# Performance work log

Measured on AMD Instinct MI355X. Metric: run time of the kernel, lower is better.

Reference implementation:

```python
import jax, jax.numpy as jnp
import numpy as np

N = 250_000          # total event nodes across the batch
E = 1_000_000        # directed edges (radius-graph style, avg degree 4)
B = 25               # graphs in the batch
BS = N // B          # nodes per graph (contiguous blocks)
NX, NY = 8, 9        # ceil(120/16), ceil(100/12) voxel cells for MaxPooling
NC = NX * NY         # 72 voxel cells per graph
M = B * NC           # pooled node slots (empty cells kept but masked)
GRIDS = 16           # MaxPoolingX: 4x4 cells of size (30,25) over 120x100
NOUT = 2
EPS = 1e-5


def spline_basis(p):
    # SplineConv basis: kernel_size=2 per dim, degree=1 open B-spline, dim=3.
    # basis_s(p) = prod_d (p_d if bit_d(s) else 1 - p_d), s = b0 + 2*b1 + 4*b2
    p = jnp.clip(p, 0.0, 1.0)
    cols = []
    for s in range(8):
        w = jnp.ones(p.shape[0], p.dtype)
        for d in range(3):
            w = w * (p[:, d] if (s >> d) & 1 else 1.0 - p[:, d])
        cols.append(w)
    return jnp.stack(cols, axis=1)  # [E, 8]


def spline_conv(x, src, dst, basis, W, emask, num_nodes):
    # SplineConv with aggr='mean', bias=False, root_weight=False
    xj = x[src]                                   # [E, Cin] gather
    msg = jnp.zeros((xj.shape[0], W.shape[2]), x.dtype)
    for s in range(W.shape[0]):                   # 8 kernel weight matrices
        msg = msg + basis[:, s:s + 1] * (xj @ W[s])
    msg = msg * emask[:, None]
    out = jax.ops.segment_sum(msg, dst, num_segments=num_nodes)
    deg = jax.ops.segment_sum(emask, dst, num_segments=num_nodes)
    return out / jnp.maximum(deg, 1.0)[:, None]


def batch_norm(x, gamma, beta, mask=None):
    # BatchNorm1d over nodes (training-mode batch statistics, biased var)
    if mask is None:
        mean = x.mean(axis=0)
        var = jnp.mean((x - mean) ** 2, axis=0)
        return (x - mean) * jax.lax.rsqrt(var + EPS) * gamma + beta
    m = mask.astype(x.dtype)[:, None]
    cnt = jnp.maximum(m.sum(), 1.0)
    mean = (x * m).sum(axis=0) / cnt
    var = (((x - mean) ** 2) * m).sum(axis=0) / cnt
    return ((x - mean) * jax.lax.rsqrt(var + EPS) * gamma + beta) * m


def _forward(x, pos, edge_attr, ws, gs, bs, fc_w, edge_index, batch):
    src, dst = edge_index[0], edge_index[1]
    basis = spline_basis(edge_attr)
    em = jnp.ones((src.shape[0],), x.dtype)
    for i in range(5):  # conv1..conv5 + norm + relu on the full event graph
        x = spline_conv(x, src, dst, basis, ws[i], em, N)
        x = jax.nn.relu(batch_norm(x, gs[i], bs[i]))
    # ---- MaxPooling: voxel grid (16,12) over pos[:, :2], coarsen graph ----
    cx = jnp.clip(jnp.floor(pos[:, 0] / 16.0).astype(jnp.int32), 0, NX - 1)
    cy = jnp.clip(jnp.floor(pos[:, 1] / 12.0).astype(jnp.int32), 0, NY - 1)
    cluster = batch * NC + cy * NX + cx           # [N] -> [0, M)
    cnt = jax.ops.segment_sum(jnp.ones((N,), x.dtype), cluster, num_segments=M)
    nmask = cnt > 0                               # non-empty voxel cells
    xp = jax.ops.segment_max(x, cluster, num_segments=M)
    xp = jnp.where(nmask[:, None], xp, 0.0)       # [M, 32]
    pp = jax.ops.segment_sum(pos, cluster, num_segments=M) / jnp.maximum(cnt, 1.0)[:, None]
    # coarsen edges: remap via cluster, drop self loops, coalesce duplicates
    key = cluster[src] * M + cluster[dst]
    key = jnp.where(cluster[src] == cluster[dst], M * M, key)
    ks = jnp.sort(key)
    dup = jnp.concatenate([jnp.zeros((1,), bool), ks[1:] == ks[:-1]])
    evalid = (ks < M * M) & (~dup)
    rs = jnp.where(evalid, ks // M, 0)
    cs = jnp.where(evalid, ks % M, 0)
    emf = evalid.astype(x.dtype)
    # Cartesian(norm=True, cat=False) on pooled positions
    d = (pp[cs] - pp[rs]) * emf[:, None]
    maxv = jnp.maximum(jnp.max(jnp.abs(d)), 1e-9)
    ea2 = d / (2.0 * maxv) + 0.5
    basis2 = spline_basis(ea2)
    for i in range(5, 7):  # conv6, conv7 on pooled graph
        xp = spline_conv(xp, rs, cs, basis2, ws[i], emf, M)
        xp = jax.nn.relu(batch_norm(xp, gs[i], bs[i], nmask))
    # ---- MaxPoolingX: (30,25) voxel grid -> 4x4 = 16 cells per graph ----
    bcl = jnp.arange(M, dtype=jnp.int32) // NC    # batch id of each cluster
    gx = jnp.clip(jnp.floor(pp[:, 0] / 30.0).astype(jnp.int32), 0, 3)
    gy = jnp.clip(jnp.floor(pp[:, 1] / 25.0).astype(jnp.int32), 0, 3)
    seg = jnp.where(nmask, bcl * GRIDS + gy * 4 + gx, B * GRIDS)
    xg = jax.ops.segment_max(xp, seg, num_segments=B * GRIDS + 1)[:B * GRIDS]
    xg = jnp.where(jnp.isfinite(xg), xg, 0.0)     # empty cells -> 0
    feat = xg.reshape(B, GRIDS * 32)              # [B, 512]
    return feat @ fc_w.T                          # [B, NOUT]


def setup_inputs() -> dict:
    key = jax.random.key(0)
    k = jax.random.split(key, 16)
    x = jax.random.uniform(k[0], (N, 1), dtype=jnp.float32)
    pos = jax.random.uniform(k[1], (N, 3), dtype=jnp.float32) * jnp.array([120.0, 100.0, 1.0], jnp.float32)
    batch = (jnp.arange(N) // BS).astype(jnp.int32)
    src = jax.random.randint(k[2], (E,), 0, N, dtype=jnp.int32)
    dst = (src // BS) * BS + jax.random.randint(k[3], (E,), 0, BS, dtype=jnp.int32)
    edge_index = jnp.stack([src, dst])
    edge_attr = jax.random.uniform(k[4], (E, 3), dtype=jnp.float32)
    chans = [1, 8, 16, 16, 16, 32, 32, 32]
    inp = {"x": x, "pos": pos, "edge_attr": edge_attr}
    for i in range(7):
        cin, cout = chans[i], chans[i + 1]
        inp[f"w{i+1}"] = jax.random.normal(k[5 + i], (8, cin, cout), jnp.float32) / np.sqrt(8.0 * cin)
    for i in range(7):
        inp[f"g{i+1}"] = jnp.ones((chans[i + 1],), jnp.float32)
    for i in range(7):
        inp[f"b{i+1}"] = jnp.zeros((chans[i + 1],), jnp.float32)
    inp["fc_w"] = jax.random.normal(k[12], (NOUT, GRIDS * 32), jnp.float32) * 0.05
    inp["edge_index"] = edge_index
    inp["batch"] = batch
    return inp


def reference(x, pos, edge_attr, w1, w2, w3, w4, w5, w6, w7,
              g1, g2, g3, g4, g5, g6, g7,
              b1, b2, b3, b4, b5, b6, b7, fc_w, edge_index, batch):
    ws = (w1, w2, w3, w4, w5, w6, w7)
    gs = (g1, g2, g3, g4, g5, g6, g7)
    bs = (b1, b2, b3, b4, b5, b6, b7)
    return _forward(x, pos, edge_attr, ws, gs, bs, fc_w, edge_index, batch)
```

## Files before the change

### kernel.cpp

```cpp
#include <hip/hip_runtime.h>

constexpr int NN   = 250000;
constexpr int NE   = 1000000;
constexpr int NBm  = 25;
constexpr int BSg  = NN / NBm;
constexpr int NCc  = 72;
constexpr int MM   = NBm * NCc;
constexpr int PRES = NBm * NCc * NCc;
constexpr int NBK  = NBm * 16;
constexpr float EPSbn = 1e-5f;


__global__ __launch_bounds__(256) void k_deg(const int* __restrict__ dst, int* __restrict__ deg, int n) {
    int e = blockIdx.x * 256 + threadIdx.x;
    if (e < n) atomicAdd(&deg[dst[e]], 1);
}

__global__ __launch_bounds__(256) void k_dhist(const int* __restrict__ deg, const int* __restrict__ batch,
                                               int* __restrict__ dhist, int n) {
    __shared__ int h[NBK];
    int tid = threadIdx.x;
    for (int i = tid; i < NBK; i += 256) h[i] = 0;
    __syncthreads();
    int i = blockIdx.x * 256 + tid;
    if (i < n) atomicAdd(&h[batch[i] * 16 + (15 - min(deg[i], 15))], 1);
    __syncthreads();
    for (int b = tid; b < NBK; b += 256) if (h[b]) atomicAdd(&dhist[b], h[b]);
}

__global__ __launch_bounds__(256) void k_dscan(const int* __restrict__ dhist, int* __restrict__ dcur) {
    __shared__ int tmp[NBK];
    int t = threadIdx.x;
    for (int i = t; i < NBK; i += 256) tmp[i] = dhist[i];
    __syncthreads();
    if (t == 0) { int run = 0; for (int i = 0; i < NBK; i++) { int v = tmp[i]; tmp[i] = run; run += v; } }
    __syncthreads();
    for (int i = t; i < NBK; i += 256) dcur[i] = tmp[i];
}

__global__ __launch_bounds__(256) void k_dscat(const int* __restrict__ deg, const int* __restrict__ batch,
                                               const float* __restrict__ x_in,
                                               int* __restrict__ dcur, int* __restrict__ pinv,
                                               int* __restrict__ deg_p, float* __restrict__ xin_p, int n) {
    __shared__ int lcnt[NBK];
    __shared__ int gbase[NBK];
    int tid = threadIdx.x;
    for (int i = tid; i < NBK; i += 256) lcnt[i] = 0;
    __syncthreads();
    int i = blockIdx.x * 256 + tid;
    int b = 0, rank = 0;
    if (i < n) {
        b = batch[i] * 16 + (15 - min(deg[i], 15));
        rank = atomicAdd(&lcnt[b], 1);
    }
    __syncthreads();
    for (int k = tid; k < NBK; k += 256)
        if (lcnt[k]) gbase[k] = atomicAdd(&dcur[k], lcnt[k]);
    __syncthreads();
    if (i < n) {
        int slot = gbase[b] + rank;
        pinv[i] = slot;
        deg_p[slot] = deg[i];
        xin_p[slot] = x_in[i];
    }
}

__global__ __launch_bounds__(256) void k_scan1(const int* __restrict__ in, int n,
                                               int* __restrict__ outEx, int* __restrict__ bsum) {
    __shared__ int lds[256];
    int t = threadIdx.x;
    int base = blockIdx.x * 2048;
    int v[8]; int s = 0;
#pragma unroll
    for (int i = 0; i < 8; i++) { int idx = base + t * 8 + i; v[i] = (idx < n) ? in[idx] : 0; s += v[i]; }
    lds[t] = s; __syncthreads();
    for (int o = 1; o < 256; o <<= 1) {
        int x = (t >= o) ? lds[t - o] : 0; __syncthreads();
        lds[t] += x; __syncthreads();
    }
    if (t == 255) bsum[blockIdx.x] = lds[255];
    int run = lds[t] - s;
#pragma unroll
    for (int i = 0; i < 8; i++) { int idx = base + t * 8 + i; if (idx < n) outEx[idx] = run; run += v[i]; }
}

__global__ __launch_bounds__(256) void k_scan2(int* bsum, int nb) {
    __shared__ int l[256];
    int t = threadIdx.x;
    int v = (t < nb) ? bsum[t] : 0;
    l[t] = v; __syncthreads();
    for (int o = 1; o < 256; o <<= 1) {
        int x = (t >= o) ? l[t - o] : 0; __syncthreads();
        l[t] += x; __syncthreads();
    }
    if (t < nb) bsum[t] = l[t] - v;
}

__global__ __launch_bounds__(256) void k_scan3(int* __restrict__ outEx, int n, const int* __restrict__ bsum) {
    int i = blockIdx.x * 256 + threadIdx.x;
    if (i < n) outEx[i] += bsum[i >> 11];
}

__global__ __launch_bounds__(256) void k_scatter(const int* __restrict__ src, const int* __restrict__ dst,
                                                 const float* __restrict__ ea, const int* __restrict__ offx,
                                                 const int* __restrict__ pinv,
                                                 int* __restrict__ cursor, float4* __restrict__ erec, int n) {
    int e = blockIdx.x * 256 + threadIdx.x;
    if (e >= n) return;
    int d = pinv[dst[e]];
    int j = offx[d] + atomicAdd(&cursor[d], 1);
    float p0 = fminf(fmaxf(ea[e * 3 + 0], 0.f), 1.f);
    float p1 = fminf(fmaxf(ea[e * 3 + 1], 0.f), 1.f);
    float p2 = fminf(fmaxf(ea[e * 3 + 2], 0.f), 1.f);
    erec[j] = make_float4(__int_as_float(pinv[src[e]]), p0, p1, p2);
}

__global__ __launch_bounds__(256) void k_cluster(const float* __restrict__ pos, const int* __restrict__ pinv,
                                                 int* __restrict__ cluster, int* __restrict__ cluster_p,
                                                 int* __restrict__ cnt, float* __restrict__ ppsum) {
    __shared__ int lcnt[NCc];
    __shared__ float lpp[NCc * 3];
    int tid = threadIdx.x;
    int g = blockIdx.x >> 3, part = blockIdx.x & 7;
    for (int i = tid; i < NCc; i += 256) lcnt[i] = 0;
    for (int i = tid; i < NCc * 3; i += 256) lpp[i] = 0.f;
    __syncthreads();
    int base = g * BSg + part * (BSg / 8);
    int lim = BSg / 8;
    for (int k = tid; k < lim; k += 256) {
        int i = base + k;
        float px = pos[i * 3], py = pos[i * 3 + 1], pz = pos[i * 3 + 2];
        int cx = min(max((int)floorf(px / 16.f), 0), 7);
        int cy = min(max((int)floorf(py / 12.f), 0), 8);
        int lc = cy * 8 + cx;
        cluster[i] = g * NCc + lc;
        cluster_p[pinv[i]] = g * NCc + lc;
        atomicAdd(&lcnt[lc], 1);
        atomicAdd(&lpp[lc * 3 + 0], px);
        atomicAdd(&lpp[lc * 3 + 1], py);
        atomicAdd(&lpp[lc * 3 + 2], pz);
    }
    __syncthreads();
    for (int c = tid; c < NCc; c += 256) {
        if (lcnt[c]) {
            atomicAdd(&cnt[g * NCc + c], lcnt[c]);
            atomicAdd(&ppsum[(g * NCc + c) * 3 + 0], lpp[c * 3 + 0]);
            atomicAdd(&ppsum[(g * NCc + c) * 3 + 1], lpp[c * 3 + 1]);
            atomicAdd(&ppsum[(g * NCc + c) * 3 + 2], lpp[c * 3 + 2]);
        }
    }
}

__global__ __launch_bounds__(256) void k_coarse(const int* __restrict__ src, const int* __restrict__ dst,
                                                const int* __restrict__ cluster, unsigned char* __restrict__ presence,
                                                int n) {
    int e = blockIdx.x * 256 + threadIdx.x;
    if (e >= n) return;
    int r = cluster[src[e]], c = cluster[dst[e]];
    if (r == c) return;
    int g = r / NCc;
    presence[g * (NCc * NCc) + (r % NCc) * NCc + (c % NCc)] = 1;
}

__global__ __launch_bounds__(256) void k_fpp(const int* __restrict__ cnt, const float* __restrict__ ppsum,
                                             float* __restrict__ pp, int* __restrict__ nmask, int* __restrict__ nmc) {
    int m = blockIdx.x * 256 + threadIdx.x;
    if (m >= MM) return;
    int c = cnt[m];
    float inv = 1.f / (float)max(c, 1);
    pp[m * 3 + 0] = ppsum[m * 3 + 0] * inv;
    pp[m * 3 + 1] = ppsum[m * 3 + 1] * inv;
    pp[m * 3 + 2] = ppsum[m * 3 + 2] * inv;
    nmask[m] = (c > 0);
    if (c > 0) atomicAdd(nmc, 1);
}

__global__ __launch_bounds__(256) void k_maxv(const unsigned char* __restrict__ presence, const float* __restrict__ pp,
                                              float* __restrict__ maxv) {
    int i = blockIdx.x * 256 + threadIdx.x;
    float m = 0.f;
    if (i < PRES && presence[i]) {
        int g = i / (NCc * NCc), rem = i % (NCc * NCc);
        int r = g * NCc + rem / NCc, c = g * NCc + rem % NCc;
        float d0 = fabsf(pp[c * 3 + 0] - pp[r * 3 + 0]);
        float d1 = fabsf(pp[c * 3 + 1] - pp[r * 3 + 1]);
        float d2 = fabsf(pp[c * 3 + 2] - pp[r * 3 + 2]);
        m = fmaxf(fmaxf(d0, d1), d2);
    }
    for (int o = 32; o; o >>= 1) m = fmaxf(m, __shfl_xor(m, o));
    if ((threadIdx.x & 63) == 0) atomicMax((int*)maxv, __float_as_int(m));
}


template <int CIN, int COUT, int TPN, bool BN>
__global__ __launch_bounds__(256) void k_conv(
    const float* __restrict__ x, const float4* __restrict__ erec,
    const int* __restrict__ off, const int* __restrict__ deg,
    const float* __restrict__ W, const float* __restrict__ st,
    const float* __restrict__ gam, const float* __restrict__ bet, float invcnt,
    float* __restrict__ out, float* __restrict__ stG, int nwaves) {
    constexpr int CPT = CIN / TPN;
    constexpr int SLICE = COUT + 4;
    constexpr int NPW = 128 / TPN;
    constexpr int CPG = (BSg + NPW - 1) / NPW;
    constexpr int WPG = (CPG + 1) / 2;
    constexpr int NH = (COUT > 16) ? 2 : 1;
    constexpr int OH = COUT / NH;
    constexpr int CWH = OH / TPN;
    __shared__ float Ws[8 * CIN * SLICE];
    __shared__ float ssum[COUT], ssq[COUT];
    int tid = threadIdx.x;
    for (int idx = tid; idx < 8 * CIN * COUT; idx += 256) {
        int s = idx / (CIN * COUT), r = idx % (CIN * COUT);
        int ci = r / COUT, co = r % COUT;
        int t_ = ci / CPT, i_ = ci % CPT;
        Ws[((s * CPT + i_) * TPN + t_) * SLICE + co] = W[idx];
    }
    if (tid < COUT) { ssum[tid] = 0.f; ssq[tid] = 0.f; }
    __syncthreads();

    int w = blockIdx.x * 4 + (tid >> 6);
    int lane = tid & 63;
    int t = lane & (TPN - 1);
    int qi = lane / TPN;
    bool wact = (w < nwaves);
    int g = wact ? (w / WPG) : 0;
    int p = wact ? (w % WPG) : 0;

    float sc[CPT], sh[CPT];
    if constexpr (BN) {
#pragma unroll
        for (int i = 0; i < CPT; i++) {
            int c = t * CPT + i;
            float mean = st[c] * invcnt;
            float var = st[CIN + c] * invcnt - mean * mean;
            float s = rsqrtf(var + EPSbn) * gam[c];
            sc[i] = s; sh[i] = bet[c] - mean * s;
        }
    }

    for (int rep = 0; rep < 2; rep++) {
        if (!wact) break;
        int c = rep ? (CPG - 1 - p) : p;
        if (rep && c == p) break;
        int base = g * BSg + c * NPW;
        int lim = min(NPW, BSg - c * NPW);
        int no = 2 * qi;
        bool act = no < lim;
        int n0 = base + no;

        float agg[2][8 * CPT];
#pragma unroll
        for (int r = 0; r < 2; r++)
#pragma unroll
            for (int i = 0; i < 8 * CPT; i++) agg[r][i] = 0.f;

        int dg0 = 0, dg1 = 0, jb0 = 0, jb1 = 0;
        if (act) {
            jb0 = off[n0];     dg0 = deg[n0];
            jb1 = off[n0 + 1]; dg1 = deg[n0 + 1];
        }
        int mx = max(dg0, dg1);
        int cl0 = max(dg0 - 1, 0), cl1 = max(dg1 - 1, 0);
        float4 rec0 = erec[min(jb0, NE - 1)];
        float4 rec1 = erec[min(jb1, NE - 1)];
        float4 nrec0 = erec[jb0 + min(1, cl0)];
        float4 nrec1 = erec[jb1 + min(1, cl1)];
        float xc0[CPT], xc1[CPT];
        {
            const float* xs0 = &x[(size_t)__float_as_int(rec0.x) * CIN + t * CPT];
            const float* xs1 = &x[(size_t)__float_as_int(rec1.x) * CIN + t * CPT];
            if constexpr (CPT == 4) {
                float4 v0 = *(const float4*)xs0; float4 v1 = *(const float4*)xs1;
                xc0[0] = v0.x; xc0[1] = v0.y; xc0[2] = v0.z; xc0[3] = v0.w;
                xc1[0] = v1.x; xc1[1] = v1.y; xc1[2] = v1.z; xc1[3] = v1.w;
            } else if constexpr (CPT == 8) {
#pragma unroll
                for (int i = 0; i < 8; i += 4) {
                    float4 v0 = *(const float4*)&xs0[i]; float4 v1 = *(const float4*)&xs1[i];
                    xc0[i] = v0.x; xc0[i + 1] = v0.y; xc0[i + 2] = v0.z; xc0[i + 3] = v0.w;
                    xc1[i] = v1.x; xc1[i + 1] = v1.y; xc1[i + 2] = v1.z; xc1[i + 3] = v1.w;
                }
            } else {
#pragma unroll
                for (int i = 0; i < CPT; i++) { xc0[i] = xs0[i]; xc1[i] = xs1[i]; }
            }
        }
        for (int m = 0; m < mx; m++) {
            float xn0[CPT], xn1[CPT];
            {
                const float* xs0 = &x[(size_t)__float_as_int(nrec0.x) * CIN + t * CPT];
                const float* xs1 = &x[(size_t)__float_as_int(nrec1.x) * CIN + t * CPT];
                if constexpr (CPT == 4) {
                    float4 v0 = *(const float4*)xs0; float4 v1 = *(const float4*)xs1;
                    xn0[0] = v0.x; xn0[1] = v0.y; xn0[2] = v0.z; xn0[3] = v0.w;
                    xn1[0] = v1.x; xn1[1] = v1.y; xn1[2] = v1.z; xn1[3] = v1.w;
                } else if constexpr (CPT == 8) {
#pragma unroll
                    for (int i = 0; i < 8; i += 4) {
                        float4 v0 = *(const float4*)&xs0[i]; float4 v1 = *(const float4*)&xs1[i];
                        xn0[i] = v0.x; xn0[i + 1] = v0.y; xn0[i + 2] = v0.z; xn0[i + 3] = v0.w;
                        xn1[i] = v1.x; xn1[i + 1] = v1.y; xn1[i + 2] = v1.z; xn1[i + 3] = v1.w;
                    }
                } else {
#pragma unroll
                    for (int i = 0; i < CPT; i++) { xn0[i] = xs0[i]; xn1[i] = xs1[i]; }
                }
            }
            float4 nn0 = erec[jb0 + min(m + 2, cl0)];
            float4 nn1 = erec[jb1 + min(m + 2, cl1)];
            float f0 = (m < dg0) ? 1.f : 0.f;
            float f1 = (m < dg1) ? 1.f : 0.f;
            float xv0[CPT], xv1[CPT];
#pragma unroll
            for (int i = 0; i < CPT; i++) { xv0[i] = xc0[i]; xv1[i] = xc1[i]; }
            if constexpr (BN) {
#pragma unroll
                for (int i = 0; i < CPT; i++) {
                    float a = xv0[i] * sc[i] + sh[i]; xv0[i] = a > 0.f ? a : 0.f;
                    float b = xv1[i] * sc[i] + sh[i]; xv1[i] = b > 0.f ? b : 0.f;
                }
            }
            {
                float p0 = rec0.y, p1 = rec0.z;
                float p2 = rec0.w * f0, q2 = (1.f - rec0.w) * f0;
                float q0 = 1.f - p0, q1 = 1.f - p1;
                float a00 = q0 * q1, a10 = p0 * q1, a01 = q0 * p1, a11 = p0 * p1;
                float bbv[8] = {a00 * q2, a10 * q2, a01 * q2, a11 * q2,
                                a00 * p2, a10 * p2, a01 * p2, a11 * p2};
#pragma unroll
                for (int k = 0; k < 8; k++)
#pragma unroll
                    for (int i = 0; i < CPT; i++) agg[0][k * CPT + i] += bbv[k] * xv0[i];
            }
            {
                float p0 = rec1.y, p1 = rec1.z;
                float p2 = rec1.w * f1, q2 = (1.f - rec1.w) * f1;
                float q0 = 1.f - p0, q1 = 1.f - p1;
                float a00 = q0 * q1, a10 = p0 * q1, a01 = q0 * p1, a11 = p0 * p1;
                float bbv[8] = {a00 * q2, a10 * q2, a01 * q2, a11 * q2,
                                a00 * p2, a10 * p2, a01 * p2, a11 * p2};
#pragma unroll
                for (int k = 0; k < 8; k++)
#pragma unroll
                    for (int i = 0; i < CPT; i++) agg[1][k * CPT + i] += bbv[k] * xv1[i];
            }
            rec0 = nrec0; rec1 = nrec1;
            nrec0 = nn0; nrec1 = nn1;
#pragma unroll
            for (int i = 0; i < CPT; i++) { xc0[i] = xn0[i]; xc1[i] = xn1[i]; }
        }

        float inv0 = 1.f / (float)max(dg0, 1);
        float inv1 = 1.f / (float)max(dg1, 1);

#pragma unroll
        for (int h = 0; h < NH; h++) {
            float o0[OH], o1[OH];
#pragma unroll
            for (int c2 = 0; c2 < OH; c2++) { o0[c2] = 0.f; o1[c2] = 0.f; }
#pragma unroll
            for (int k = 0; k < 8; k++)
#pragma unroll
                for (int i = 0; i < CPT; i++) {
                    float a0 = agg[0][k * CPT + i];
                    float a1 = agg[1][k * CPT + i];
                    const float4* wr = (const float4*)&Ws[((k * CPT + i) * TPN + t) * SLICE + h * OH];
#pragma unroll
                    for (int c2 = 0; c2 < OH / 4; c2++) {
                        float4 wv = wr[c2];
                        o0[4 * c2 + 0] += a0 * wv.x; o0[4 * c2 + 1] += a0 * wv.y;
                        o0[4 * c2 + 2] += a0 * wv.z; o0[4 * c2 + 3] += a0 * wv.w;
                        o1[4 * c2 + 0] += a1 * wv.x; o1[4 * c2 + 1] += a1 * wv.y;
                        o1[4 * c2 + 2] += a1 * wv.z; o1[4 * c2 + 3] += a1 * wv.w;
                    }
                }
#pragma unroll
            for (int m = 1; m < TPN; m <<= 1)
#pragma unroll
                for (int c2 = 0; c2 < OH; c2++) { o0[c2] += __shfl_xor(o0[c2], m); o1[c2] += __shfl_xor(o1[c2], m); }

            float v0[CWH], v1[CWH], sv[CWH], qv[CWH];
#pragma unroll
            for (int c2 = 0; c2 < CWH; c2++) {
                v0[c2] = act ? o0[t * CWH + c2] * inv0 : 0.f;
                v1[c2] = act ? o1[t * CWH + c2] * inv1 : 0.f;
                sv[c2] = v0[c2] + v1[c2];
                qv[c2] = v0[c2] * v0[c2] + v1[c2] * v1[c2];
            }
            if (act) {
                float* op0 = &out[(size_t)n0 * COUT + h * OH + t * CWH];
                float* op1 = op0 + COUT;
#pragma unroll
                for (int c2 = 0; c2 < CWH; c2++) { op0[c2] = v0[c2]; op1[c2] = v1[c2]; }
            }
#pragma unroll
            for (int m = TPN; m < 64; m <<= 1)
#pragma unroll
                for (int c2 = 0; c2 < CWH; c2++) { sv[c2] += __shfl_xor(sv[c2], m); qv[c2] += __shfl_xor(qv[c2], m); }
            if (lane < TPN) {
#pragma unroll
                for (int c2 = 0; c2 < CWH; c2++) {
                    atomicAdd(&ssum[h * OH + t * CWH + c2], sv[c2]);
                    atomicAdd(&ssq[h * OH + t * CWH + c2], qv[c2]);
                }
            }
        }
    }
    __syncthreads();
    if (tid < COUT) atomicAdd(&stG[tid], ssum[tid]);
    else if (tid < 2 * COUT) atomicAdd(&stG[tid], ssq[tid - COUT]);
}

__global__ __launch_bounds__(256) void k_pool(const float* __restrict__ x, const int* __restrict__ cluster_p,
                                              const float* __restrict__ st, const float* __restrict__ gam,
                                              const float* __restrict__ bet, float invcnt,
                                              float* __restrict__ xp) {
    __shared__ float cellv[NCc * 32];
    __shared__ float scs[32], shs[32];
    int tid = threadIdx.x;
    int g = blockIdx.x >> 3, part = blockIdx.x & 7;
    for (int i = tid; i < NCc * 32; i += 256) cellv[i] = 0.f;
    if (tid < 32) {
        float mean = st[tid] * invcnt;
        float var = st[32 + tid] * invcnt - mean * mean;
        float s = rsqrtf(var + EPSbn) * gam[tid];
        scs[tid] = s; shs[tid] = bet[tid] - mean * s;
    }
    __syncthreads();
    int base = g * BSg + part * (BSg / 8);
    const int nelem = (BSg / 8) * 32;
    for (int ii = tid; ii < nelem; ii += 256) {
        int nd = base + (ii >> 5), ch = ii & 31;
        float v = x[(size_t)nd * 32 + ch] * scs[ch] + shs[ch];
        v = v > 0.f ? v : 0.f;
        int lc = cluster_p[nd] - g * NCc;
        atomicMax((int*)&cellv[lc * 32 + ch], __float_as_int(v));
    }
    __syncthreads();
    for (int ii = tid; ii < NCc * 32; ii += 256)
        atomicMax((int*)&xp[g * NCc * 32 + ii], __float_as_int(cellv[ii]));
}

__global__ __launch_bounds__(256) void k_y(const float* __restrict__ xp, const float* __restrict__ W,
                                           float* __restrict__ y) {
    int i = blockIdx.x * 256 + threadIdx.x;
    if (i >= MM * 256) return;
    int r = i >> 8, rem = i & 255, s = rem >> 5, co = rem & 31;
    const float* xr = &xp[r * 32];
    const float* w = &W[s * 1024 + co];
    float a = 0.f;
#pragma unroll
    for (int ci = 0; ci < 32; ci++) a += xr[ci] * w[ci * 32];
    y[i] = a;
}

__global__ __launch_bounds__(256) void k_y2(const float* __restrict__ pt, const float* __restrict__ W,
                                            const float* __restrict__ st, const float* __restrict__ gam,
                                            const float* __restrict__ bet, const int* __restrict__ nmask,
                                            const int* __restrict__ nmc, float* __restrict__ y) {
    __shared__ float scs[32], shs[32];
    int tid = threadIdx.x;
    if (tid < 32) {
        float cntf = (float)max(nmc[0], 1);
        float mean = st[tid] / cntf;
        float var = st[32 + tid] / cntf - mean * mean;
        float s = rsqrtf(var + EPSbn) * gam[tid];
        scs[tid] = s; shs[tid] = bet[tid] - mean * s;
    }
    __syncthreads();
    int i = blockIdx.x * 256 + tid;
    if (i >= MM * 256) return;
    int r = i >> 8, rem = i & 255, s = rem >> 5, co = rem & 31;
    float a = 0.f;
    if (nmask[r]) {
        const float* xr = &pt[r * 32];
        const float* w = &W[s * 1024 + co];
#pragma unroll
        for (int ci = 0; ci < 32; ci++) {
            float v = xr[ci] * scs[ci] + shs[ci];
            v = v > 0.f ? v : 0.f;
            a += v * w[ci * 32];
        }
    }
    y[i] = a;
}

__global__ __launch_bounds__(256) void k_convp(const float* __restrict__ y, const float* __restrict__ pp,
                                               const unsigned char* __restrict__ presence,
                                               const float* __restrict__ maxv, float* __restrict__ out,
                                               float* __restrict__ stG) {
    __shared__ float ssum[32], ssq[32];
    int tid = threadIdx.x;
    if (tid < 32) { ssum[tid] = 0.f; ssq[tid] = 0.f; }
    __syncthreads();
    int i = blockIdx.x * 256 + tid;
    int c = i >> 5, co = i & 31;
    int g = c / NCc, lc = c % NCc;
    float mv = fmaxf(maxv[0], 1e-9f);
    float inv2 = 0.5f / mv;
    float pcx = pp[c * 3], pcy = pp[c * 3 + 1], pcz = pp[c * 3 + 2];
    const unsigned char* pr = &presence[g * (NCc * NCc) + lc];
    float acc = 0.f; int dg = 0;
    for (int lr = 0; lr < NCc; lr++) {
        if (pr[lr * NCc]) {
            dg++;
            int r = g * NCc + lr;
            float p0 = fminf(fmaxf((pcx - pp[r * 3]) * inv2 + 0.5f, 0.f), 1.f);
            float p1 = fminf(fmaxf((pcy - pp[r * 3 + 1]) * inv2 + 0.5f, 0.f), 1.f);
            float p2 = fminf(fmaxf((pcz - pp[r * 3 + 2]) * inv2 + 0.5f, 0.f), 1.f);
            float q0 = 1.f - p0, q1 = 1.f - p1, q2 = 1.f - p2;
            const float* yr = &y[r * 256 + co];
            acc += (q0 * q1 * q2) * yr[0]   + (p0 * q1 * q2) * yr[32]
                 + (q0 * p1 * q2) * yr[64]  + (p0 * p1 * q2) * yr[96]
                 + (q0 * q1 * p2) * yr[128] + (p0 * q1 * p2) * yr[160]
                 + (q0 * p1 * p2) * yr[192] + (p0 * p1 * p2) * yr[224];
        }
    }
    float val = acc / (float)max(dg, 1);
    out[i] = val;
    float sv = val, qv = val * val;
    sv += __shfl_xor(sv, 32); qv += __shfl_xor(qv, 32);
    int lane = tid & 63;
    if (lane < 32) { atomicAdd(&ssum[lane], sv); atomicAdd(&ssq[lane], qv); }
    __syncthreads();
    if (tid < 32) atomicAdd(&stG[tid], ssum[tid]);
    else if (tid < 64) atomicAdd(&stG[32 + tid - 32], ssq[tid - 32]);
}

__global__ __launch_bounds__(256) void k_poolX(const float* __restrict__ pt, const float* __restrict__ pp,
                                               const float* __restrict__ st, const float* __restrict__ gam,
                                               const float* __restrict__ bet, const int* __restrict__ nmask,
                                               const int* __restrict__ nmc, float* __restrict__ xg) {
    int i = blockIdx.x * 256 + threadIdx.x;
    if (i >= MM * 32) return;
    int m = i >> 5, ch = i & 31;
    if (!nmask[m]) return;
    float cntf = (float)max(nmc[0], 1);
    float mean = st[ch] / cntf;
    float var = st[32 + ch] / cntf - mean * mean;
    float s = rsqrtf(var + EPSbn) * gam[ch];
    float v = pt[i] * s + (bet[ch] - mean * s);
    v = v > 0.f ? v : 0.f;
    int g = m / NCc;
    int gx = min(max((int)floorf(pp[m * 3] / 30.f), 0), 3);
    int gy = min(max((int)floorf(pp[m * 3 + 1] / 25.f), 0), 3);
    int seg = g * 16 + gy * 4 + gx;
    atomicMax((int*)&xg[seg * 32 + ch], __float_as_int(v));
}

__global__ __launch_bounds__(64) void k_fc(const float* __restrict__ xg, const float* __restrict__ fcw,
                                           float* __restrict__ out) {
    int q = blockIdx.x;
    int b = q >> 1, o = q & 1;
    int l = threadIdx.x;
    float a = 0.f;
    for (int k = l; k < 512; k += 64) a += xg[b * 512 + k] * fcw[o * 512 + k];
    for (int s = 32; s; s >>= 1) a += __shfl_xor(a, s);
    if (l == 0) out[b * 2 + o] = a;
}


extern "C" void kernel_launch(void* const* d_in, const int* in_sizes, int n_in,
                              void* d_out, int out_size, void* d_ws, size_t ws_size,
                              hipStream_t stream) {
    const float* x_in  = (const float*)d_in[0];
    const float* pos   = (const float*)d_in[1];
    const float* eattr = (const float*)d_in[2];
    const float* w[7];  for (int i = 0; i < 7; i++) w[i]  = (const float*)d_in[3 + i];
    const float* gm[7]; for (int i = 0; i < 7; i++) gm[i] = (const float*)d_in[10 + i];
    const float* bt[7]; for (int i = 0; i < 7; i++) bt[i] = (const float*)d_in[17 + i];
    const float* fcw   = (const float*)d_in[24];
    const int* ei      = (const int*)d_in[25];
    const int* batch   = (const int*)d_in[26];
    const int* esrc = ei;
    const int* edst = ei + NE;
    float* outp = (float*)d_out;

    char* base = (char*)d_ws;
    size_t cur = 0;
    auto alloc = [&](size_t elems) -> void* {
        void* p = base + cur;
        cur += (((elems * 4) + 255) & ~(size_t)255);
        return p;
    };
    int*   deg_i     = (int*)alloc(NN);
    int*   cursor    = (int*)alloc(NN);
    int*   cnt_i     = (int*)alloc(MM);
    float* ppsum     = (float*)alloc(MM * 3);
    unsigned char* presence = (unsigned char*)alloc(PRES / 4);
    float* maxv      = (float*)alloc(64);
    int*   nmc       = (int*)alloc(64);
    int*   dhist     = (int*)alloc(NBK);
    float* st        = (float*)alloc(7 * 64);
    float* xp_pool   = (float*)alloc(MM * 32);
    float* xg        = (float*)alloc(NBm * 16 * 32);
    size_t zero_bytes = cur;
    int*   off_ex    = (int*)alloc(NN);
    int*   bsum      = (int*)alloc(256);
    int*   cluster   = (int*)alloc(NN);
    int*   cluster_p = (int*)alloc(NN);
    int*   dcur      = (int*)alloc(NBK);
    int*   pinv      = (int*)alloc(NN);
    int*   deg_p     = (int*)alloc(NN);
    float* xin_p     = (float*)alloc(NN);
    float4* erec     = (float4*)alloc((size_t)NE * 4);
    float* x_a       = (float*)alloc((size_t)NN * 32);
    float* x_b       = (float*)alloc((size_t)NN * 16);
    float* pp        = (float*)alloc(MM * 3);
    int*   nmask     = (int*)alloc(MM);
    float* ybuf      = (float*)alloc(MM * 256);
    float* pt0       = (float*)alloc(MM * 32);
    float* pt1       = (float*)alloc(MM * 32);
    (void)ws_size; (void)in_sizes; (void)n_in; (void)out_size;

    (void)hipMemsetAsync(d_ws, 0, zero_bytes, stream);

    int gE = (NE + 255) / 256;
    int gN = (NN + 255) / 256;
    int nbS = (NN + 2047) / 2048;

    k_deg<<<gE, 256, 0, stream>>>(edst, deg_i, NE);
    k_dhist<<<gN, 256, 0, stream>>>(deg_i, batch, dhist, NN);
    k_dscan<<<1, 256, 0, stream>>>(dhist, dcur);
    k_dscat<<<gN, 256, 0, stream>>>(deg_i, batch, x_in, dcur, pinv, deg_p, xin_p, NN);
    k_scan1<<<nbS, 256, 0, stream>>>(deg_p, NN, off_ex, bsum);
    k_scan2<<<1, 256, 0, stream>>>(bsum, nbS);
    k_scan3<<<gN, 256, 0, stream>>>(off_ex, NN, bsum);
    k_scatter<<<gE, 256, 0, stream>>>(esrc, edst, eattr, off_ex, pinv, cursor, erec, NE);
    k_cluster<<<NBm * 8, 256, 0, stream>>>(pos, pinv, cluster, cluster_p, cnt_i, ppsum);
    k_coarse<<<gE, 256, 0, stream>>>(esrc, edst, cluster, presence, NE);
    k_fpp<<<(MM + 255) / 256, 256, 0, stream>>>(cnt_i, ppsum, pp, nmask, nmc);
    k_maxv<<<(PRES + 255) / 256, 256, 0, stream>>>(presence, pp, maxv);

    const float invN = 1.f / (float)NN;
    constexpr int W1 = NBm * ((((BSg + 127) / 128) + 1) / 2);
    constexpr int W2 = NBm * ((((BSg + 63) / 64) + 1) / 2);
    constexpr int W4 = NBm * ((((BSg + 31) / 32) + 1) / 2);
    k_conv<1, 8, 1, false><<<(W1 + 3) / 4, 256, 0, stream>>>(xin_p, erec, off_ex, deg_p,
                                                             w[0], nullptr, nullptr, nullptr, 0.f, x_a, st + 0, W1);
    k_conv<8, 16, 2, true><<<(W2 + 3) / 4, 256, 0, stream>>>(x_a, erec, off_ex, deg_p,
                                                             w[1], st + 0, gm[0], bt[0], invN, x_b, st + 64, W2);
    k_conv<16, 16, 4, true><<<(W4 + 3) / 4, 256, 0, stream>>>(x_b, erec, off_ex, deg_p,
                                                              w[2], st + 64, gm[1], bt[1], invN, x_a, st + 128, W4);
    k_conv<16, 16, 4, true><<<(W4 + 3) / 4, 256, 0, stream>>>(x_a, erec, off_ex, deg_p,
                                                              w[3], st + 128, gm[2], bt[2], invN, x_b, st + 192, W4);
    k_conv<16, 32, 4, true><<<(W4 + 3) / 4, 256, 0, stream>>>(x_b, erec, off_ex, deg_p,
                                                              w[4], st + 192, gm[3], bt[3], invN, x_a, st + 256, W4);
    k_pool<<<NBm * 8, 256, 0, stream>>>(x_a, cluster_p, st + 256, gm[4], bt[4], invN, xp_pool);
    k_y<<<(MM * 256 + 255) / 256, 256, 0, stream>>>(xp_pool, w[5], ybuf);
    k_convp<<<(MM * 32) / 256, 256, 0, stream>>>(ybuf, pp, presence, maxv, pt0, st + 320);
    k_y2<<<(MM * 256 + 255) / 256, 256, 0, stream>>>(pt0, w[6], st + 320, gm[5], bt[5], nmask, nmc, ybuf);
    k_convp<<<(MM * 32) / 256, 256, 0, stream>>>(ybuf, pp, presence, maxv, pt1, st + 384);
    k_poolX<<<(MM * 32 + 255) / 256, 256, 0, stream>>>(pt1, pp, st + 384, gm[6], bt[6], nmask, nmc, xg);
    k_fc<<<50, 64, 0, stream>>>(xg, fcw, outp);
}
```

Before: 630.0 us.

## Fuse edge scatter with coarse presence, shrink conv blocks, drop x prefetch

Merges the edge scatter and coarse-graph presence kernels into one pass over the edges, so src/dst are read once and one launch is removed. Halves the conv blocks to 128 threads (two waves each), which gives more blocks and spreads the shared weight staging, but each block now loads the weight tile for fewer waves. Removes the software pipelining of neighbor feature gathers in the conv loop. This lowers register pressure but exposes gather latency on every edge iteration.

```diff
diff --git a/kernel.cpp b/kernel.cpp
--- a/kernel.cpp
+++ b/kernel.cpp
@@ -99,20 +99,6 @@
 __global__ __launch_bounds__(256) void k_scan3(int* __restrict__ outEx, int n, const int* __restrict__ bsum) {
     int i = blockIdx.x * 256 + threadIdx.x;
     if (i < n) outEx[i] += bsum[i >> 11];
-}
-
-__global__ __launch_bounds__(256) void k_scatter(const int* __restrict__ src, const int* __restrict__ dst,
-                                                 const float* __restrict__ ea, const int* __restrict__ offx,
-                                                 const int* __restrict__ pinv,
-                                                 int* __restrict__ cursor, float4* __restrict__ erec, int n) {
-    int e = blockIdx.x * 256 + threadIdx.x;
-    if (e >= n) return;
-    int d = pinv[dst[e]];
-    int j = offx[d] + atomicAdd(&cursor[d], 1);
-    float p0 = fminf(fmaxf(ea[e * 3 + 0], 0.f), 1.f);
-    float p1 = fminf(fmaxf(ea[e * 3 + 1], 0.f), 1.f);
-    float p2 = fminf(fmaxf(ea[e * 3 + 2], 0.f), 1.f);
-    erec[j] = make_float4(__int_as_float(pinv[src[e]]), p0, p1, p2);
 }
 
 __global__ __launch_bounds__(256) void k_cluster(const float* __restrict__ pos, const int* __restrict__ pinv,
@@ -151,15 +137,25 @@
     }
 }
 
-__global__ __launch_bounds__(256) void k_coarse(const int* __restrict__ src, const int* __restrict__ dst,
-                                                const int* __restrict__ cluster, unsigned char* __restrict__ presence,
-                                                int n) {
+__global__ __launch_bounds__(256) void k_scatter(const int* __restrict__ src, const int* __restrict__ dst,
+                                                 const float* __restrict__ ea, const int* __restrict__ offx,
+                                                 const int* __restrict__ pinv, const int* __restrict__ cluster,
+                                                 int* __restrict__ cursor, float4* __restrict__ erec,
+                                                 unsigned char* __restrict__ presence, int n) {
     int e = blockIdx.x * 256 + threadIdx.x;
     if (e >= n) return;
-    int r = cluster[src[e]], c = cluster[dst[e]];
-    if (r == c) return;
-    int g = r / NCc;
-    presence[g * (NCc * NCc) + (r % NCc) * NCc + (c % NCc)] = 1;
+    int s = src[e], d = dst[e];
+    int pd = pinv[d];
+    int j = offx[pd] + atomicAdd(&cursor[pd], 1);
+    float p0 = fminf(fmaxf(ea[e * 3 + 0], 0.f), 1.f);
+    float p1 = fminf(fmaxf(ea[e * 3 + 1], 0.f), 1.f);
+    float p2 = fminf(fmaxf(ea[e * 3 + 2], 0.f), 1.f);
+    erec[j] = make_float4(__int_as_float(pinv[s]), p0, p1, p2);
+    int r = cluster[s], c = cluster[d];
+    if (r != c) {
+        int g = r / NCc;
+        presence[g * (NCc * NCc) + (r % NCc) * NCc + (c % NCc)] = 1;
+    }
 }
 
 __global__ __launch_bounds__(256) void k_fpp(const int* __restrict__ cnt, const float* __restrict__ ppsum,
@@ -193,7 +189,7 @@
 
 
 template <int CIN, int COUT, int TPN, bool BN>
-__global__ __launch_bounds__(256) void k_conv(
+__global__ __launch_bounds__(128) void k_conv(
     const float* __restrict__ x, const float4* __restrict__ erec,
     const int* __restrict__ off, const int* __restrict__ deg,
     const float* __restrict__ W, const float* __restrict__ st,
@@ -210,7 +206,7 @@
     __shared__ float Ws[8 * CIN * SLICE];
     __shared__ float ssum[COUT], ssq[COUT];
     int tid = threadIdx.x;
-    for (int idx = tid; idx < 8 * CIN * COUT; idx += 256) {
+    for (int idx = tid; idx < 8 * CIN * COUT; idx += 128) {
         int s = idx / (CIN * COUT), r = idx % (CIN * COUT);
         int ci = r / COUT, co = r % COUT;
         int t_ = ci / CPT, i_ = ci % CPT;
@@ -219,7 +215,7 @@
     if (tid < COUT) { ssum[tid] = 0.f; ssq[tid] = 0.f; }
     __syncthreads();
 
-    int w = blockIdx.x * 4 + (tid >> 6);
+    int w = blockIdx.x * 2 + (tid >> 6);
     int lane = tid & 63;
     int t = lane & (TPN - 1);
     int qi = lane / TPN;
@@ -264,56 +260,33 @@
         int cl0 = max(dg0 - 1, 0), cl1 = max(dg1 - 1, 0);
         float4 rec0 = erec[min(jb0, NE - 1)];
         float4 rec1 = erec[min(jb1, NE - 1)];
-        float4 nrec0 = erec[jb0 + min(1, cl0)];
-        float4 nrec1 = erec[jb1 + min(1, cl1)];
-        float xc0[CPT], xc1[CPT];
-        {
-            const float* xs0 = &x[(size_t)__float_as_int(rec0.x) * CIN + t * CPT];
-            const float* xs1 = &x[(size_t)__float_as_int(rec1.x) * CIN + t * CPT];
+        for (int m = 0; m < mx; m++) {
+            int s0 = __float_as_int(rec0.x);
+            int s1 = __float_as_int(rec1.x);
+            const float* xs0 = &x[(size_t)s0 * CIN + t * CPT];
+            const float* xs1 = &x[(size_t)s1 * CIN + t * CPT];
+            float xv0[CPT], xv1[CPT];
             if constexpr (CPT == 4) {
-                float4 v0 = *(const float4*)xs0; float4 v1 = *(const float4*)xs1;
-                xc0[0] = v0.x; xc0[1] = v0.y; xc0[2] = v0.z; xc0[3] = v0.w;
-                xc1[0] = v1.x; xc1[1] = v1.y; xc1[2] = v1.z; xc1[3] = v1.w;
+                float4 v0 = *(const float4*)xs0;
+                float4 v1 = *(const float4*)xs1;
+                xv0[0] = v0.x; xv0[1] = v0.y; xv0[2] = v0.z; xv0[3] = v0.w;
+                xv1[0] = v1.x; xv1[1] = v1.y; xv1[2] = v1.z; xv1[3] = v1.w;
             } else if constexpr (CPT == 8) {
 #pragma unroll
                 for (int i = 0; i < 8; i += 4) {
-                    float4 v0 = *(const float4*)&xs0[i]; float4 v1 = *(const float4*)&xs1[i];
-                    xc0[i] = v0.x; xc0[i + 1] = v0.y; xc0[i + 2] = v0.z; xc0[i + 3] = v0.w;
-                    xc1[i] = v1.x; xc1[i + 1] = v1.y; xc1[i + 2] = v1.z; xc1[i + 3] = v1.w;
+                    float4 v0 = *(const float4*)&xs0[i];
+                    float4 v1 = *(const float4*)&xs1[i];
+                    xv0[i] = v0.x; xv0[i + 1] = v0.y; xv0[i + 2] = v0.z; xv0[i + 3] = v0.w;
+                    xv1[i] = v1.x; xv1[i + 1] = v1.y; xv1[i + 2] = v1.z; xv1[i + 3] = v1.w;
                 }
             } else {
 #pragma unroll
-                for (int i = 0; i < CPT; i++) { xc0[i] = xs0[i]; xc1[i] = xs1[i]; }
+                for (int i = 0; i < CPT; i++) { xv0[i] = xs0[i]; xv1[i] = xs1[i]; }
             }
-        }
-        for (int m = 0; m < mx; m++) {
-            float xn0[CPT], xn1[CPT];
-            {
-                const float* xs0 = &x[(size_t)__float_as_int(nrec0.x) * CIN + t * CPT];
-                const float* xs1 = &x[(size_t)__float_as_int(nrec1.x) * CIN + t * CPT];
-                if constexpr (CPT == 4) {
-                    float4 v0 = *(const float4*)xs0; float4 v1 = *(const float4*)xs1;
-                    xn0[0] = v0.x; xn0[1] = v0.y; xn0[2] = v0.z; xn0[3] = v0.w;
-                    xn1[0] = v1.x; xn1[1] = v1.y; xn1[2] = v1.z; xn1[3] = v1.w;
-                } else if constexpr (CPT == 8) {
-#pragma unroll
-                    for (int i = 0; i < 8; i += 4) {
-                        float4 v0 = *(const float4*)&xs0[i]; float4 v1 = *(const float4*)&xs1[i];
-                        xn0[i] = v0.x; xn0[i + 1] = v0.y; xn0[i + 2] = v0.z; xn0[i + 3] = v0.w;
-                        xn1[i] = v1.x; xn1[i + 1] = v1.y; xn1[i + 2] = v1.z; xn1[i + 3] = v1.w;
-                    }
-                } else {
-#pragma unroll
-                    for (int i = 0; i < CPT; i++) { xn0[i] = xs0[i]; xn1[i] = xs1[i]; }
-                }
-            }
-            float4 nn0 = erec[jb0 + min(m + 2, cl0)];
-            float4 nn1 = erec[jb1 + min(m + 2, cl1)];
+            float4 nrec0 = erec[jb0 + min(m + 1, cl0)];
+            float4 nrec1 = erec[jb1 + min(m + 1, cl1)];
             float f0 = (m < dg0) ? 1.f : 0.f;
             float f1 = (m < dg1) ? 1.f : 0.f;
-            float xv0[CPT], xv1[CPT];
-#pragma unroll
-            for (int i = 0; i < CPT; i++) { xv0[i] = xc0[i]; xv1[i] = xc1[i]; }
             if constexpr (BN) {
 #pragma unroll
                 for (int i = 0; i < CPT; i++) {
@@ -346,9 +319,6 @@
                     for (int i = 0; i < CPT; i++) agg[1][k * CPT + i] += bbv[k] * xv1[i];
             }
             rec0 = nrec0; rec1 = nrec1;
-            nrec0 = nn0; nrec1 = nn1;
-#pragma unroll
-            for (int i = 0; i < CPT; i++) { xc0[i] = xn0[i]; xc1[i] = xn1[i]; }
         }
 
         float inv0 = 1.f / (float)max(dg0, 1);
@@ -627,9 +597,8 @@
     k_scan1<<<nbS, 256, 0, stream>>>(deg_p, NN, off_ex, bsum);
     k_scan2<<<1, 256, 0, stream>>>(bsum, nbS);
     k_scan3<<<gN, 256, 0, stream>>>(off_ex, NN, bsum);
-    k_scatter<<<gE, 256, 0, stream>>>(esrc, edst, eattr, off_ex, pinv, cursor, erec, NE);
     k_cluster<<<NBm * 8, 256, 0, stream>>>(pos, pinv, cluster, cluster_p, cnt_i, ppsum);
-    k_coarse<<<gE, 256, 0, stream>>>(esrc, edst, cluster, presence, NE);
+    k_scatter<<<gE, 256, 0, stream>>>(esrc, edst, eattr, off_ex, pinv, cluster, cursor, erec, presence, NE);
     k_fpp<<<(MM + 255) / 256, 256, 0, stream>>>(cnt_i, ppsum, pp, nmask, nmc);
     k_maxv<<<(PRES + 255) / 256, 256, 0, stream>>>(presence, pp, maxv);
 
@@ -637,15 +606,15 @@
     constexpr int W1 = NBm * ((((BSg + 127) / 128) + 1) / 2);
     constexpr int W2 = NBm * ((((BSg + 63) / 64) + 1) / 2);
     constexpr int W4 = NBm * ((((BSg + 31) / 32) + 1) / 2);
-    k_conv<1, 8, 1, false><<<(W1 + 3) / 4, 256, 0, stream>>>(xin_p, erec, off_ex, deg_p,
+    k_conv<1, 8, 1, false><<<(W1 + 1) / 2, 128, 0, stream>>>(xin_p, erec, off_ex, deg_p,
                                                              w[0], nullptr, nullptr, nullptr, 0.f, x_a, st + 0, W1);
-    k_conv<8, 16, 2, true><<<(W2 + 3) / 4, 256, 0, stream>>>(x_a, erec, off_ex, deg_p,
+    k_conv<8, 16, 2, true><<<(W2 + 1) / 2, 128, 0, stream>>>(x_a, erec, off_ex, deg_p,
                                                              w[1], st + 0, gm[0], bt[0], invN, x_b, st + 64, W2);
-    k_conv<16, 16, 4, true><<<(W4 + 3) / 4, 256, 0, stream>>>(x_b, erec, off_ex, deg_p,
+    k_conv<16, 16, 4, true><<<(W4 + 1) / 2, 128, 0, stream>>>(x_b, erec, off_ex, deg_p,
                                                               w[2], st + 64, gm[1], bt[1], invN, x_a, st + 128, W4);
-    k_conv<16, 16, 4, true><<<(W4 + 3) / 4, 256, 0, stream>>>(x_a, erec, off_ex, deg_p,
+    k_conv<16, 16, 4, true><<<(W4 + 1) / 2, 128, 0, stream>>>(x_a, erec, off_ex, deg_p,
                                                               w[3], st + 128, gm[2], bt[2], invN, x_b, st + 192, W4);
-    k_conv<16, 32, 4, true><<<(W4 + 3) / 4, 256, 0, stream>>>(x_b, erec, off_ex, deg_p,
+    k_conv<16, 32, 4, true><<<(W4 + 1) / 2, 128, 0, stream>>>(x_b, erec, off_ex, deg_p,
                                                               w[4], st + 192, gm[3], bt[3], invN, x_a, st + 256, W4);
     k_pool<<<NBm * 8, 256, 0, stream>>>(x_a, cluster_p, st + 256, gm[4], bt[4], invN, xp_pool);
     k_y<<<(MM * 256 + 255) / 256, 256, 0, stream>>>(xp_pool, w[5], ybuf);
```

Result: slower. 671.9 us (+6.7%).
